# Kernel optimization log

Hardware: AMD Instinct MI355X
Metric: run time of the kernel (lower is better)

Reference implementation:

```python
import jax, jax.numpy as jnp
import numpy as np

N_NODES = 50000


def gcn_conv(x, W, b, src, dst, n_nodes):
    """PyG-style GCNConv: add self-loops, symmetric deg^-1/2 norm, linear, aggregate."""
    # add self-loops
    loop = jnp.arange(n_nodes, dtype=src.dtype)
    s = jnp.concatenate([src, loop])  # source (j)
    d = jnp.concatenate([dst, loop])  # target (i)
    # degree computed on target index (PyG: deg = scatter ones over col)
    deg = jax.ops.segment_sum(jnp.ones_like(d, dtype=x.dtype), d, num_segments=n_nodes)
    dinv = jnp.where(deg > 0, jax.lax.rsqrt(deg), 0.0)
    norm = dinv[s] * dinv[d]  # [E+N]
    h = x @ W  # [N, out]
    msg = h[s] * norm[:, None]  # gather + scale, [E+N, out]
    out = jax.ops.segment_sum(msg, d, num_segments=n_nodes)  # scatter-add
    return out + b


def setup_inputs() -> dict:
    key = jax.random.key(0)
    k1, k2, k3, k4 = jax.random.split(key, 4)
    hidden = 128
    in_dim = hidden + 2
    E = 800000
    x = jax.random.normal(k1, (N_NODES, in_dim), dtype=jnp.float32)
    edge_index = jax.random.randint(k2, (2, E), 0, N_NODES, dtype=jnp.int64)
    # Glorot-ish init for weights
    W1 = jax.random.normal(k3, (in_dim, hidden), dtype=jnp.float32) / np.sqrt(in_dim)
    W2 = jax.random.normal(k4, (hidden, hidden), dtype=jnp.float32) / np.sqrt(hidden)
    b1 = jnp.zeros((hidden,), dtype=jnp.float32)
    b2 = jnp.zeros((hidden,), dtype=jnp.float32)
    return {"x": x, "edge_index": edge_index, "W1": W1, "b1": b1, "W2": W2, "b2": b2}


def reference(x, edge_index, W1, b1, W2, b2):
    src, dst = edge_index[0], edge_index[1]
    h = gcn_conv(x, W1, b1, src, dst, N_NODES)
    h = jax.nn.relu(h)
    h = gcn_conv(h, W2, b2, src, dst, N_NODES)
    h = jax.nn.relu(h)
    return h
```

## Files before the change

kernel.cpp:

```cpp
#include <hip/hip_runtime.h>
#include <hip/hip_fp16.h>


#define NNODES 50000


__global__ void count_kernel(const int* __restrict__ dst, int* __restrict__ cnt, int E) {
    int e = blockIdx.x * blockDim.x + threadIdx.x;
    if (e < E) atomicAdd(&cnt[dst[e]], 1);
}

__global__ __launch_bounds__(256) void scan_blocksum(const int* __restrict__ cnt,
                                                     int* __restrict__ bsum, int N) {
    __shared__ int ws[4];
    int i = blockIdx.x * 256 + threadIdx.x;
    int v = (i < N) ? cnt[i] : 0;
#pragma unroll
    for (int off = 1; off < 64; off <<= 1) v += __shfl_xor(v, off);
    int lane = threadIdx.x & 63, w = threadIdx.x >> 6;
    if (lane == 0) ws[w] = v;
    __syncthreads();
    if (threadIdx.x == 0) bsum[blockIdx.x] = ws[0] + ws[1] + ws[2] + ws[3];
}

__global__ __launch_bounds__(256) void scan_partials(const int* __restrict__ bsum,
                                                     int* __restrict__ boff,
                                                     int* __restrict__ row_start,
                                                     int NB, int N) {
    __shared__ int ws[4];
    int t = threadIdx.x;
    int v = (t < NB) ? bsum[t] : 0;
    int lane = t & 63, w = t >> 6;
    int inc = v;
#pragma unroll
    for (int off = 1; off < 64; off <<= 1) {
        int n = __shfl_up(inc, off);
        if (lane >= off) inc += n;
    }
    if (lane == 63) ws[w] = inc;
    __syncthreads();
    int woff = 0;
    for (int k = 0; k < w; ++k) woff += ws[k];
    int excl = woff + inc - v;
    if (t < NB) boff[t] = excl;
    if (t == NB - 1) row_start[N] = excl + v;
}

__global__ __launch_bounds__(256) void scan_final(const int* __restrict__ cnt,
                                                  const int* __restrict__ boff,
                                                  int* __restrict__ row_start,
                                                  float* __restrict__ dinv, int N) {
    __shared__ int ws[4];
    int i = blockIdx.x * 256 + threadIdx.x;
    int v = (i < N) ? cnt[i] : 0;
    int lane = threadIdx.x & 63, w = threadIdx.x >> 6;
    int inc = v;
#pragma unroll
    for (int off = 1; off < 64; off <<= 1) {
        int n = __shfl_up(inc, off);
        if (lane >= off) inc += n;
    }
    if (lane == 63) ws[w] = inc;
    __syncthreads();
    int woff = 0;
    for (int k = 0; k < w; ++k) woff += ws[k];
    if (i < N) {
        row_start[i] = boff[blockIdx.x] + woff + inc - v;
        dinv[i] = rsqrtf((float)(v + 1));
    }
}

__global__ __launch_bounds__(256) void scatter_kernel(const int* __restrict__ src,
                                                      const int* __restrict__ dst,
                                                      const int* __restrict__ row_start,
                                                      int* __restrict__ cursor,
                                                      int* __restrict__ esrc,
                                                      int E, int npo) {
    int owner = blockIdx.x & 7;
    int nblk  = gridDim.x >> 3;
    int bo    = blockIdx.x >> 3;
    int lo = owner * npo;
    int hi = lo + npo;
    for (int e = bo * 256 + threadIdx.x; e < E; e += nblk * 256) {
        int d = dst[e];
        if (d >= lo && d < hi) {
            int p = row_start[d] + atomicAdd(&cursor[d], 1);
            esrc[p] = src[e];
        }
    }
}


__global__ __launch_bounds__(256) void gemm_kernel(const float* __restrict__ A,
                                                   const float* __restrict__ W,
                                                   const float* __restrict__ dinv,
                                                   __half* __restrict__ Hs,
                                                   int M, int K) {
    constexpr int BM = 64, BN = 128, BK = 32, LDA = BK + 2;
    __shared__ float sA[BM * LDA];
    __shared__ float sW[BK][BN];
    int t = threadIdx.x;
    int row0 = blockIdx.x * BM;
    int tx = t & 15;
    int ty = t >> 4;
    float acc[4][8] = {};

    for (int k0 = 0; k0 < K; k0 += BK) {
#pragma unroll
        for (int j = 0; j < 4; ++j) {
            int s  = t + 256 * j;
            int r  = s >> 4;
            int c2 = s & 15;
            int gr = row0 + r;
            int gk = k0 + c2 * 2;
            float2 v = make_float2(0.f, 0.f);
            if (gr < M) {
                if (gk + 1 < K)      v = *reinterpret_cast<const float2*>(&A[(size_t)gr * K + gk]);
                else if (gk < K)     v.x = A[(size_t)gr * K + gk];
            }
            *reinterpret_cast<float2*>(&sA[r * LDA + c2 * 2]) = v;
        }
#pragma unroll
        for (int j = 0; j < 4; ++j) {
            int s  = t + 256 * j;
            int r  = s >> 5;
            int c4 = s & 31;
            int gk = k0 + r;
            float4 v = make_float4(0.f, 0.f, 0.f, 0.f);
            if (gk < K) v = *reinterpret_cast<const float4*>(&W[(size_t)gk * BN + c4 * 4]);
            *reinterpret_cast<float4*>(&sW[r][c4 * 4]) = v;
        }
        __syncthreads();
#pragma unroll 4
        for (int kk = 0; kk < BK; ++kk) {
            float4 b0 = *reinterpret_cast<const float4*>(&sW[kk][tx * 4]);
            float4 b1 = *reinterpret_cast<const float4*>(&sW[kk][64 + tx * 4]);
            float a[4];
#pragma unroll
            for (int i = 0; i < 4; ++i) a[i] = sA[(ty * 4 + i) * LDA + kk];
#pragma unroll
            for (int i = 0; i < 4; ++i) {
                acc[i][0] = fmaf(a[i], b0.x, acc[i][0]);
                acc[i][1] = fmaf(a[i], b0.y, acc[i][1]);
                acc[i][2] = fmaf(a[i], b0.z, acc[i][2]);
                acc[i][3] = fmaf(a[i], b0.w, acc[i][3]);
                acc[i][4] = fmaf(a[i], b1.x, acc[i][4]);
                acc[i][5] = fmaf(a[i], b1.y, acc[i][5]);
                acc[i][6] = fmaf(a[i], b1.z, acc[i][6]);
                acc[i][7] = fmaf(a[i], b1.w, acc[i][7]);
            }
        }
        __syncthreads();
    }
#pragma unroll
    for (int i = 0; i < 4; ++i) {
        int gr = row0 + ty * 4 + i;
        if (gr < M) {
            float di = dinv[gr];
            __half2 p0 = __floats2half2_rn(di * acc[i][0], di * acc[i][1]);
            __half2 p1 = __floats2half2_rn(di * acc[i][2], di * acc[i][3]);
            __half2 p2 = __floats2half2_rn(di * acc[i][4], di * acc[i][5]);
            __half2 p3 = __floats2half2_rn(di * acc[i][6], di * acc[i][7]);
            uint2 pk0, pk1;
            pk0.x = *reinterpret_cast<unsigned int*>(&p0);
            pk0.y = *reinterpret_cast<unsigned int*>(&p1);
            pk1.x = *reinterpret_cast<unsigned int*>(&p2);
            pk1.y = *reinterpret_cast<unsigned int*>(&p3);
            *reinterpret_cast<uint2*>(&Hs[(size_t)gr * BN + tx * 4])      = pk0;
            *reinterpret_cast<uint2*>(&Hs[(size_t)gr * BN + 64 + tx * 4]) = pk1;
        }
    }
}


__global__ __launch_bounds__(128) void agg_kernel(const __half* __restrict__ Hs,
                                                  const int* __restrict__ row_start,
                                                  const int* __restrict__ esrc,
                                                  const float* __restrict__ dinv,
                                                  const float* __restrict__ bias,
                                                  float* __restrict__ out, int N) {
    constexpr int F = 128;
    __shared__ int s_idx[128];
    int i = blockIdx.x;
    int f = threadIdx.x;
    int beg = row_start[i];
    int end = row_start[i + 1];
    float acc0 = 0.f, acc1 = 0.f;
    for (int base = beg; base < end; base += 128) {
        int m = end - base; if (m > 128) m = 128;
        __syncthreads();
        if (f < m) s_idx[f] = esrc[base + f];
        __syncthreads();
        int j = 0;
        for (; j + 4 <= m; j += 4) {
            float v0 = __half2float(Hs[(size_t)s_idx[j + 0] * F + f]);
            float v1 = __half2float(Hs[(size_t)s_idx[j + 1] * F + f]);
            float v2 = __half2float(Hs[(size_t)s_idx[j + 2] * F + f]);
            float v3 = __half2float(Hs[(size_t)s_idx[j + 3] * F + f]);
            acc0 += v0 + v2;
            acc1 += v1 + v3;
        }
        for (; j < m; ++j)
            acc0 += __half2float(Hs[(size_t)s_idx[j] * F + f]);
    }
    float self = __half2float(Hs[(size_t)i * F + f]);
    float v = fmaf(dinv[i], acc0 + acc1 + self, bias[f]);
    out[(size_t)i * F + f] = fmaxf(v, 0.f);
}


extern "C" void kernel_launch(void* const* d_in, const int* in_sizes, int n_in,
                              void* d_out, int out_size, void* d_ws, size_t ws_size,
                              hipStream_t stream) {
    const float* x  = (const float*)d_in[0];
    const int*   ei = (const int*)d_in[1];
    const float* W1 = (const float*)d_in[2];
    const float* b1 = (const float*)d_in[3];
    const float* W2 = (const float*)d_in[4];
    const float* b2 = (const float*)d_in[5];

    const int N   = NNODES;
    const int E   = in_sizes[1] / 2;
    const int K1  = in_sizes[0] / N;
    const int HID = in_sizes[3];
    const int NB  = (N + 255) / 256;
    const int NPO = (N + 7) / 8;

    const int* src = ei;
    const int* dst = ei + E;

    int*    cnt       = (int*)d_ws;
    int*    cursor    = cnt + N;
    int*    row_start = cursor + N;
    float*  dinv      = (float*)(row_start + N + 4);
    int*    bsum      = (int*)(dinv + N);
    int*    boff      = bsum + 256;
    int*    esrc      = boff + 256;
    __half* Hs        = (__half*)(esrc + E);
    float*  outf      = (float*)d_out;

    hipMemsetAsync(cnt, 0, sizeof(int) * 2 * (size_t)N, stream);

    count_kernel<<<(E + 255) / 256, 256, 0, stream>>>(dst, cnt, E);
    scan_blocksum<<<NB, 256, 0, stream>>>(cnt, bsum, N);
    scan_partials<<<1, 256, 0, stream>>>(bsum, boff, row_start, NB, N);
    scan_final<<<NB, 256, 0, stream>>>(cnt, boff, row_start, dinv, N);
    scatter_kernel<<<2048, 256, 0, stream>>>(src, dst, row_start, cursor, esrc, E, NPO);

    gemm_kernel<<<(N + 63) / 64, 256, 0, stream>>>(x, W1, dinv, Hs, N, K1);
    agg_kernel<<<N, 128, 0, stream>>>(Hs, row_start, esrc, dinv, b1, outf, N);
    gemm_kernel<<<(N + 63) / 64, 256, 0, stream>>>(outf, W2, dinv, Hs, N, HID);
    agg_kernel<<<N, 128, 0, stream>>>(Hs, row_start, esrc, dinv, b2, outf, N);
}
```

Before: 327.2 us.

## Aggregate one node per wavefront with vectorized half loads and shuffle-broadcast indices

Rewrites the aggregation kernel so each 64-lane wavefront handles one node, with two half-wavefronts each taking alternate edges and every lane loading 4 halves (8 bytes) per row. Neighbor indices are prefetched into a register and broadcast with shuffles instead of staged in shared memory, which removes the __syncthreads barriers. The two halves' partial sums are combined with a cross-lane xor shuffle, and the output is written as float4. This cuts block count, narrow 2-byte loads and barrier overhead, but the per-iteration branch and possible divergence on the degree bound remain.

```diff
diff --git a/kernel.cpp b/kernel.cpp
--- a/kernel.cpp
+++ b/kernel.cpp
@@ -173,39 +173,58 @@
 }
 
 
-__global__ __launch_bounds__(128) void agg_kernel(const __half* __restrict__ Hs,
+__global__ __launch_bounds__(256) void agg_kernel(const __half* __restrict__ Hs,
                                                   const int* __restrict__ row_start,
                                                   const int* __restrict__ esrc,
                                                   const float* __restrict__ dinv,
                                                   const float* __restrict__ bias,
                                                   float* __restrict__ out, int N) {
     constexpr int F = 128;
-    __shared__ int s_idx[128];
-    int i = blockIdx.x;
-    int f = threadIdx.x;
-    int beg = row_start[i];
-    int end = row_start[i + 1];
-    float acc0 = 0.f, acc1 = 0.f;
-    for (int base = beg; base < end; base += 128) {
-        int m = end - base; if (m > 128) m = 128;
-        __syncthreads();
-        if (f < m) s_idx[f] = esrc[base + f];
-        __syncthreads();
-        int j = 0;
-        for (; j + 4 <= m; j += 4) {
-            float v0 = __half2float(Hs[(size_t)s_idx[j + 0] * F + f]);
-            float v1 = __half2float(Hs[(size_t)s_idx[j + 1] * F + f]);
-            float v2 = __half2float(Hs[(size_t)s_idx[j + 2] * F + f]);
-            float v3 = __half2float(Hs[(size_t)s_idx[j + 3] * F + f]);
-            acc0 += v0 + v2;
-            acc1 += v1 + v3;
-        }
-        for (; j < m; ++j)
-            acc0 += __half2float(Hs[(size_t)s_idx[j] * F + f]);
-    }
-    float self = __half2float(Hs[(size_t)i * F + f]);
-    float v = fmaf(dinv[i], acc0 + acc1 + self, bias[f]);
-    out[(size_t)i * F + f] = fmaxf(v, 0.f);
+    int node = blockIdx.x * 4 + (threadIdx.x >> 6);
+    if (node >= N) return;
+    int lane = threadIdx.x & 63;
+    int c = lane & 31;
+    int h = lane >> 5;
+    int beg = row_start[node];
+    int deg = row_start[node + 1] - beg;
+
+    int spre = (lane < deg) ? esrc[beg + lane] : 0;
+
+    float a0 = 0.f, a1 = 0.f, a2 = 0.f, a3 = 0.f;
+    for (int j = 0; j < deg; j += 2) {
+        int jj = j + h;
+        int s;
+        if (jj < 64) s = __shfl(spre, jj);
+        else         s = (jj < deg) ? esrc[beg + jj] : 0;
+        if (jj < deg) {
+            uint2 v = *reinterpret_cast<const uint2*>(&Hs[(size_t)s * F + c * 4]);
+            __half2 h0 = *reinterpret_cast<__half2*>(&v.x);
+            __half2 h1 = *reinterpret_cast<__half2*>(&v.y);
+            float2 f0 = __half22float2(h0);
+            float2 f1 = __half22float2(h1);
+            a0 += f0.x; a1 += f0.y; a2 += f1.x; a3 += f1.y;
+        }
+    }
+    a0 += __shfl_xor(a0, 32);
+    a1 += __shfl_xor(a1, 32);
+    a2 += __shfl_xor(a2, 32);
+    a3 += __shfl_xor(a3, 32);
+
+    if (h == 0) {
+        uint2 sv = *reinterpret_cast<const uint2*>(&Hs[(size_t)node * F + c * 4]);
+        __half2 s0 = *reinterpret_cast<__half2*>(&sv.x);
+        __half2 s1 = *reinterpret_cast<__half2*>(&sv.y);
+        float2 g0 = __half22float2(s0);
+        float2 g1 = __half22float2(s1);
+        float4 b = *reinterpret_cast<const float4*>(&bias[c * 4]);
+        float di = dinv[node];
+        float4 r;
+        r.x = fmaxf(fmaf(di, a0 + g0.x, b.x), 0.f);
+        r.y = fmaxf(fmaf(di, a1 + g0.y, b.y), 0.f);
+        r.z = fmaxf(fmaf(di, a2 + g1.x, b.z), 0.f);
+        r.w = fmaxf(fmaf(di, a3 + g1.y, b.w), 0.f);
+        *reinterpret_cast<float4*>(&out[(size_t)node * F + c * 4]) = r;
+    }
 }
 
 
@@ -248,7 +267,7 @@
     scatter_kernel<<<2048, 256, 0, stream>>>(src, dst, row_start, cursor, esrc, E, NPO);
 
     gemm_kernel<<<(N + 63) / 64, 256, 0, stream>>>(x, W1, dinv, Hs, N, K1);
-    agg_kernel<<<N, 128, 0, stream>>>(Hs, row_start, esrc, dinv, b1, outf, N);
+    agg_kernel<<<(N + 3) / 4, 256, 0, stream>>>(Hs, row_start, esrc, dinv, b1, outf, N);
     gemm_kernel<<<(N + 63) / 64, 256, 0, stream>>>(outf, W2, dinv, Hs, N, HID);
-    agg_kernel<<<N, 128, 0, stream>>>(Hs, row_start, esrc, dinv, b2, outf, N);
-}
+    agg_kernel<<<(N + 3) / 4, 256, 0, stream>>>(Hs, row_start, esrc, dinv, b2, outf, N);
+}
```

Measured after the change: 316.7 us. -3.2%, faster.
